# Kernel optimization log

Hardware: AMD Instinct MI355X
Metric: run time of the kernel (lower is better)

Reference implementation:

```python
import jax, jax.numpy as jnp
import numpy as np
from jax import lax

DIST_THRESH = 180.0
ATT_THRESH = 0.05


def setup_inputs() -> dict:
    key = jax.random.key(0)
    ks = jax.random.split(key, 6)
    B, N, H, W = 16, 512, 25, 25
    F, Fh = H * W, int(H * W * 1.5)  # 625, 937
    x4 = jax.random.normal(ks[0], (B, N, H, W), dtype=jnp.float32) * 0.25
    attention = jax.random.uniform(ks[1], (B, N, 1, 1), dtype=jnp.float32)
    W1 = jax.random.normal(ks[2], (2, F, Fh), dtype=jnp.float32) * (1.0 / np.sqrt(F))
    b1 = jnp.zeros((Fh,), dtype=jnp.float32)
    W2 = jax.random.normal(ks[3], (2, Fh, F), dtype=jnp.float32) * (1.0 / np.sqrt(Fh))
    b2 = jnp.zeros((F,), dtype=jnp.float32)
    return {"x4": x4, "attention": attention, "W1": W1, "b1": b1, "W2": W2, "b2": b2}


def _build_adjacency(X, att):
    """X: [B,N,F] node features, att: [B,N]. Returns thresholded adjacency [B,N,N]."""
    B, N, F = X.shape
    # pairwise L1 distances, row-by-row scan to avoid materializing [B,N,N,F]
    Xs = jnp.swapaxes(X, 0, 1)  # [N,B,F]

    def row(_, xi):  # xi: [B,F]
        d = jnp.sum(jnp.abs(xi[:, None, :] - X), axis=-1)  # [B,N]
        return None, d

    _, D = lax.scan(row, None, Xs)          # [N,B,N]
    D = jnp.swapaxes(D, 0, 1)               # [B,N,N]
    att_d = jnp.abs(att[:, :, None] - att[:, None, :])  # [B,N,N]
    A = ((D <= DIST_THRESH) & (att_d <= ATT_THRESH)).astype(jnp.float32)
    # original only fills i<j and j<i, diagonal stays 0
    A = A * (1.0 - jnp.eye(N, dtype=jnp.float32))
    return A


def _process_graph(A):
    """A + I, then row-normalize by inverse degree (D^-1 (A+I))."""
    N = A.shape[1]
    A = A + jnp.eye(N, dtype=A.dtype)
    deg = jnp.sum(A, axis=-1)               # [B,N]
    dinv = jnp.where(deg > 0, 1.0 / deg, 0.0)
    return dinv[:, :, None] * A


def _cheb_conv(x, L, Wk, b):
    """ChebConv with K=2 over dense normalized graph L: T0=x, T1=Lx."""
    t1 = jnp.einsum('bij,bjf->bif', L, x)
    return jnp.einsum('bnf,fo->bno', x, Wk[0]) + jnp.einsum('bnf,fo->bno', t1, Wk[1]) + b


def reference(x4, attention, W1, b1, W2, b2):
    B, N, H, W = x4.shape
    X = x4.reshape(B, N, H * W)             # [B,N,625] flow_x
    att = attention[:, :, 0, 0]             # [B,N]
    A = _build_adjacency(X, att)
    L = _process_graph(A)
    h = jax.nn.relu(_cheb_conv(X, L, W1, b1))   # [B,N,937]
    out = jax.nn.relu(_cheb_conv(h, L, W2, b2))  # [B,N,625]
    return out
```

## Files before the change

kernel.cpp:

```cpp
#include <hip/hip_runtime.h>
#include <stdint.h>

typedef uint16_t u16;
typedef uint32_t u32;
typedef __attribute__((ext_vector_type(4))) float f32x4;
typedef __attribute__((ext_vector_type(4))) unsigned short us4;
typedef __attribute__((ext_vector_type(8))) unsigned short us8;

#define NB   16
#define NN   512
#define FF   625
#define FH   937
#define ROWS 8192
#define KS1  1280
#define KS2  1920
#define NPX  640
#define NPH  960
#define F4   160
#define GQ   4

using frag_ab = __attribute__((ext_vector_type(8))) short;
using frag_cd = __attribute__((ext_vector_type(4))) float;

__device__ __forceinline__ u16 f32_bf16(float f) {
  union { float f; uint32_t u; } x; x.f = f;
  uint32_t r = x.u + 0x7fffu + ((x.u >> 16) & 1u);
  return (u16)(r >> 16);
}
__device__ __forceinline__ void gload_lds16(const void* g, void* l) {
  __builtin_amdgcn_global_load_lds((__attribute__((address_space(1))) void*)g,
                                   (__attribute__((address_space(3))) void*)l,
                                   16, 0, 0);
}

__global__ __launch_bounds__(256) void prep(
    const float* __restrict__ x4, const float* __restrict__ att,
    const float* __restrict__ W1, const float* __restrict__ W2,
    f32x4* __restrict__ Xpad, u16* __restrict__ Xcat, u16* __restrict__ Xt,
    u16* __restrict__ W1t, u16* __restrict__ W2t,
    u16* __restrict__ order, float* __restrict__ att_s)
{
  __shared__ __align__(16) float smem[2112];
  const int blk = blockIdx.x;
  const int tid = threadIdx.x;

  if (blk < 16) {
    float* a_sh = smem;
    const int b = blk;
    a_sh[tid]       = att[b * NN + tid];
    a_sh[tid + 256] = att[b * NN + tid + 256];
    __syncthreads();
    #pragma unroll
    for (int h = 0; h < 2; ++h) {
      const int i = tid + h * 256;
      const float ai = a_sh[i];
      int r = 0;
      for (int j = 0; j < NN; ++j) {
        const float aj = a_sh[j];
        r += (aj < ai) || (aj == ai && j < i);
      }
      order[(size_t)b * NN + r] = (u16)i;
      att_s[(size_t)b * NN + r] = ai;
    }
  } else if (blk < 1040) {
    float* T = smem;
    const int idx = blk - 16;
    const int xcd = idx & 7, sub = idx >> 3;
    const int b = xcd * 2 + (sub >> 6);
    const int rr = sub & 63;
    const int q = rr >> 4;
    const int nt = rr & 15;
    const int node0 = nt * 32;
    const int tx = tid & 31, ty = tid >> 5;
    const int lrow = tid >> 3, lcol = tid & 7;

    int buf = 0;
    {
      const int f0 = q * 160;
      #pragma unroll
      for (int r = 0; r < 4; ++r) {
        const int node = node0 + ty + r * 8;
        const int f = f0 + tx;
        T[(ty + r * 8) * 33 + tx] = (f < FF) ? x4[((size_t)b * NN + node) * FF + f] : 0.f;
      }
    }
    __syncthreads();

    for (int c = 0; c < 5; ++c) {
      const int f0 = q * 160 + c * 32;
      float vnext[4];
      const bool has = (c + 1 < 5);
      if (has) {
        const int fn = f0 + 32 + tx;
        #pragma unroll
        for (int r = 0; r < 4; ++r) {
          const int node = node0 + ty + r * 8;
          vnext[r] = (fn < FF) ? x4[((size_t)b * NN + node) * FF + fn] : 0.f;
        }
      }
      {
        const int node_l = lrow, k4s = lcol;
        const size_t grow = (size_t)b * NN + node0 + node_l;
        const int k4 = q * 40 + c * 8 + k4s;
        f32x4 v; us4 o;
        #pragma unroll
        for (int t = 0; t < 4; ++t) {
          const float x = T[buf * 1056 + node_l * 33 + k4s * 4 + t];
          v[t] = x; o[t] = f32_bf16(x);
        }
        Xpad[grow * F4 + k4] = v;
        *(us4*)(Xcat + grow * KS1 + k4 * 4) = o;
      }
      {
        const int fl = lrow, nl = lcol;
        const int f = f0 + fl;
        us4 ov;
        #pragma unroll
        for (int t = 0; t < 4; ++t)
          ov[t] = f32_bf16(T[buf * 1056 + (nl * 4 + t) * 33 + fl]);
        *(us4*)(Xt + ((size_t)b * NPX + f) * 512 + node0 + nl * 4) = ov;
      }
      if (has) {
        #pragma unroll
        for (int r = 0; r < 4; ++r)
          T[(buf ^ 1) * 1056 + (ty + r * 8) * 33 + tx] = vnext[r];
        __syncthreads();
        buf ^= 1;
      }
    }
  } else if (blk < 2320) {
    float (*tile)[33] = (float(*)[33])smem;
    const int bb = blk - 1040;
    const int kt = bb % 40, nt = bb / 40;
    const int tx = tid & 31, ty = tid >> 5;
    #pragma unroll
    for (int r = 0; r < 4; ++r) {
      int k = kt * 32 + ty + r * 8;
      int n = nt * 32 + tx;
      float v = 0.f;
      int c = -1, kk = 0;
      if (k < 625) { c = 0; kk = k; }
      else if (k >= 640 && k < 1265) { c = 1; kk = k - 640; }
      if (c >= 0 && n < FH) v = W1[((size_t)c * 625 + kk) * FH + n];
      tile[ty + r * 8][tx] = v;
    }
    __syncthreads();
    #pragma unroll
    for (int r = 0; r < 4; ++r) {
      int n = nt * 32 + ty + r * 8;
      int k = kt * 32 + tx;
      W1t[(size_t)n * KS1 + k] = f32_bf16(tile[tx][ty + r * 8]);
    }
  } else {
    float (*tile)[33] = (float(*)[33])smem;
    const int bb = blk - 2320;
    const int kt = bb % 60, nt = bb / 60;
    const int tx = tid & 31, ty = tid >> 5;
    #pragma unroll
    for (int r = 0; r < 4; ++r) {
      int k = kt * 32 + ty + r * 8;
      int n = nt * 32 + tx;
      float v = 0.f;
      int c = -1, kk = 0;
      if (k < 937) { c = 0; kk = k; }
      else if (k >= 960 && k < 1897) { c = 1; kk = k - 960; }
      if (c >= 0 && n < FF) v = W2[((size_t)c * 937 + kk) * FF + n];
      tile[ty + r * 8][tx] = v;
    }
    __syncthreads();
    #pragma unroll
    for (int r = 0; r < 4; ++r) {
      int n = nt * 32 + ty + r * 8;
      int k = kt * 32 + tx;
      W2t[(size_t)n * KS2 + k] = f32_bf16(tile[tx][ty + r * 8]);
    }
  }
}

__global__ __launch_bounds__(256) void build_L(
    const f32x4* __restrict__ Xpad,
    const u16* __restrict__ order,
    const float* __restrict__ att_s,
    u16* __restrict__ L)
{
  __shared__ float atts[512];
  __shared__ u16 ords[512];
  __shared__ u16 cand[512];
  __shared__ u16 flag[GQ][512];
  __shared__ int ncand, naccs[GQ];

  const int tid = threadIdx.x;
  const int blk = blockIdx.x;
  const int xcd = blk & 7, sub = blk >> 3;
  const int b = xcd * 2 + (sub >> 7);
  const int p0 = (sub & 127) * GQ;
  const f32x4* Xb4 = Xpad + (size_t)b * NN * F4;

  atts[tid]       = att_s[b * NN + tid];
  atts[tid + 256] = att_s[b * NN + tid + 256];
  ords[tid]       = order[b * NN + tid];
  ords[tid + 256] = order[b * NN + tid + 256];
  {
    u32* fz = (u32*)&flag[0][0];
    #pragma unroll
    for (int s = 0; s < GQ; ++s) fz[tid + s * 256] = 0;
  }
  if (tid == 0) ncand = 0;
  if (tid < GQ) naccs[tid] = 0;
  __syncthreads();

  float av[GQ]; int ig[GQ];
  #pragma unroll
  for (int g = 0; g < GQ; ++g) { av[g] = atts[p0 + g]; ig[g] = ords[p0 + g]; }
  if (tid < GQ) flag[tid][ords[p0 + tid]] = 1;

  {
    const float lo = av[0] - 0.0501f, hi = av[GQ - 1] + 0.0501f;
    const bool q0 = (atts[tid] >= lo) && (atts[tid] <= hi);
    const bool q1 = (atts[tid + 256] >= lo) && (atts[tid + 256] <= hi);
    const unsigned long long m0 = __ballot(q0);
    const unsigned long long m1 = __ballot(q1);
    const int c0 = __popcll(m0);
    const int c1 = __popcll(m1);
    const int lane = tid & 63;
    int base = 0;
    if (lane == 0 && (c0 + c1)) base = atomicAdd(&ncand, c0 + c1);
    base = __shfl(base, 0, 64);
    const unsigned long long below = (1ull << lane) - 1ull;
    if (q0) cand[base + __popcll(m0 & below)] = (u16)tid;
    if (q1) cand[base + c0 + __popcll(m1 & below)] = (u16)(tid + 256);
  }
  __syncthreads();
  const int nc = ncand;

  const int hl = tid & 31;
  const int hw = tid >> 5;

  f32x4 xi[GQ][5];
  #pragma unroll
  for (int g = 0; g < GQ; ++g) {
    const f32x4* Xi = Xb4 + (size_t)ig[g] * F4;
    #pragma unroll
    for (int s = 0; s < 5; ++s) xi[g][s] = Xi[s * 32 + hl];
  }

  for (int c = hw; c < nc; c += 8) {
    const int p = cand[c];
    const int j = ords[p];
    const float aj = atts[p];
    const f32x4* Xj = Xb4 + (size_t)j * F4;
    f32x4 xj[5];
    #pragma unroll
    for (int s = 0; s < 5; ++s) xj[s] = Xj[s * 32 + hl];

    float pd[GQ];
    #pragma unroll
    for (int g = 0; g < GQ; ++g) {
      float p2 = 0.f;
      #pragma unroll
      for (int t = 0; t < 4; ++t) {
        p2 += fabsf(xi[g][0][t] - xj[0][t]) + fabsf(xi[g][1][t] - xj[1][t])
            + fabsf(xi[g][2][t] - xj[2][t]) + fabsf(xi[g][3][t] - xj[3][t])
            + fabsf(xi[g][4][t] - xj[4][t]);
      }
      pd[g] = p2;
    }
    #pragma unroll
    for (int off = 16; off; off >>= 1) {
      #pragma unroll
      for (int g = 0; g < GQ; ++g) pd[g] += __shfl_xor(pd[g], off, 64);
    }
    if (hl == 0) {
      #pragma unroll
      for (int g = 0; g < GQ; ++g) {
        if (pd[g] <= 180.0f && fabsf(av[g] - aj) <= 0.05f && j != ig[g]) {
          flag[g][j] = 1;
          atomicAdd(&naccs[g], 1);
        }
      }
    }
  }
  __syncthreads();

  #pragma unroll
  for (int g = 0; g < GQ; ++g) {
    const u16 dv = f32_bf16(1.0f / (float)(naccs[g] + 1));
    const long row = (long)b * NN + ig[g];
    const u32 lo2 = flag[g][2 * tid]     ? (u32)dv : 0u;
    const u32 hi2 = flag[g][2 * tid + 1] ? (u32)dv : 0u;
    *(u32*)(L + (size_t)row * 512 + 2 * tid) = lo2 | (hi2 << 16);
  }
}

template <int KS, int NTILE, int NREAL, int NSTORE, bool RELU, bool BIAS, bool OUT_BF16>
__device__ __forceinline__ void gemm_core(
    const u16* __restrict__ At,
    const u16* __restrict__ Btt,
    const float* __restrict__ bias, void* __restrict__ C,
    long crow0, int col0, int ldc)
{
  constexpr int NI = NTILE / 32;
  constexpr int BR = NTILE / 32;
  __shared__ __align__(16) u16 Ash[128 * 64];
  __shared__ __align__(16) u16 Bsh[NTILE * 64];

  const int tid  = threadIdx.x;
  const int lane = tid & 63;
  const int wave = tid >> 6;
  const int wm = wave & 1, wn = wave >> 1;
  const int q = lane >> 4, l16 = lane & 15;

  const u16* pa[4]; const u16* pb[BR];
  #pragma unroll
  for (int r = 0; r < 4; ++r) {
    const int ci = r * 256 + tid;
    const int row = ci >> 3, cpos = ci & 7;
    pa[r] = At + (size_t)row * KS + (cpos ^ (row & 7)) * 8;
  }
  #pragma unroll
  for (int r = 0; r < BR; ++r) {
    const int ci = r * 256 + tid;
    const int row = ci >> 3, cpos = ci & 7;
    pb[r] = Btt + (size_t)row * KS + (cpos ^ (row & 7)) * 8;
  }
  const int wbase = (tid & 192) * 8;

  const frag_ab* fA[4][2]; const frag_ab* fB[NI][2];
  #pragma unroll
  for (int mi = 0; mi < 4; ++mi) {
    const int row = wm * 64 + mi * 16 + l16;
    fA[mi][0] = (const frag_ab*)&Ash[row * 64 + ((q    ) ^ (l16 & 7)) * 8];
    fA[mi][1] = (const frag_ab*)&Ash[row * 64 + ((q + 4) ^ (l16 & 7)) * 8];
  }
  #pragma unroll
  for (int ni = 0; ni < NI; ++ni) {
    const int row = wn * (NTILE / 2) + ni * 16 + l16;
    fB[ni][0] = (const frag_ab*)&Bsh[row * 64 + ((q    ) ^ (l16 & 7)) * 8];
    fB[ni][1] = (const frag_ab*)&Bsh[row * 64 + ((q + 4) ^ (l16 & 7)) * 8];
  }

  frag_cd acc[4][NI] = {};

  constexpr int KT = KS / 64;
  for (int kt = 0; kt < KT; ++kt) {
    __syncthreads();
    #pragma unroll
    for (int r = 0; r < 4; ++r) { gload_lds16(pa[r], &Ash[r * 2048 + wbase]); pa[r] += 64; }
    #pragma unroll
    for (int r = 0; r < BR; ++r) { gload_lds16(pb[r], &Bsh[r * 2048 + wbase]); pb[r] += 64; }
    __syncthreads();

    #pragma unroll
    for (int kk = 0; kk < 2; ++kk) {
      frag_ab av[4], bv[NI];
      #pragma unroll
      for (int mi = 0; mi < 4; ++mi) av[mi] = *fA[mi][kk];
      #pragma unroll
      for (int ni = 0; ni < NI; ++ni) bv[ni] = *fB[ni][kk];
      #pragma unroll
      for (int mi = 0; mi < 4; ++mi)
        #pragma unroll
        for (int ni = 0; ni < NI; ++ni)
          acc[mi][ni] = __builtin_amdgcn_mfma_f32_16x16x32_bf16(
              av[mi], bv[ni], acc[mi][ni], 0, 0, 0);
    }
  }

  #pragma unroll
  for (int ni = 0; ni < NI; ++ni) {
    const int col = col0 + wn * (NTILE / 2) + ni * 16 + l16;
    if (col >= NSTORE) continue;
    const bool ok = (col < NREAL);
    float bvv = 0.f;
    if (BIAS) bvv = ok ? bias[col] : 0.f;
    #pragma unroll
    for (int mi = 0; mi < 4; ++mi) {
      #pragma unroll
      for (int r = 0; r < 4; ++r) {
        const long rowg = crow0 + wm * 64 + mi * 16 + q * 4 + r;
        float v = acc[mi][ni][r];
        if (BIAS) v += bvv;
        if (RELU) v = fmaxf(v, 0.f);
        if (!ok) v = 0.f;
        if (OUT_BF16) ((u16*)C)[rowg * (size_t)ldc + col] = f32_bf16(v);
        else          ((float*)C)[rowg * (size_t)ldc + col] = v;
      }
    }
  }
}

template <int KS, int NTILE, int NREAL, int NSTORE, bool RELU, bool BIAS, bool OUT_BF16>
__global__ __launch_bounds__(256) void gemm_dense(
    const u16* __restrict__ A, const u16* __restrict__ Bt,
    const float* __restrict__ bias, void* __restrict__ C, int ldc)
{
  const int x = blockIdx.x;
  const int mt = ((x & 7) << 3) | (x >> 3);
  gemm_core<KS, NTILE, NREAL, NSTORE, RELU, BIAS, OUT_BF16>(
      A + (size_t)mt * 128 * KS, Bt + (size_t)blockIdx.y * NTILE * KS,
      bias, C, (long)mt * 128, blockIdx.y * NTILE, ldc);
}

template <int NP>
__global__ __launch_bounds__(256) void spmm(
    const u16* __restrict__ L, const u16* __restrict__ Bt,
    u16* __restrict__ C, int ldc)
{
  constexpr int TPB = 4 * (NP / 64);
  const int blk = blockIdx.x;
  const int xcd = blk & 7, sub = blk >> 3;
  const int b = xcd * 2 + sub / TPB;
  const int t = sub % TPB;
  const int mt = t & 3, nt = t >> 2;
  gemm_core<512, 64, NP, NP, false, false, true>(
      L + ((size_t)b * 512 + mt * 128) * 512,
      Bt + ((size_t)b * NP + nt * 64) * 512,
      nullptr, C, (long)b * 512 + mt * 128, nt * 64, ldc);
}

__global__ __launch_bounds__(256) void transpose_h(
    const u16* __restrict__ hcat, u16* __restrict__ ht)
{
  __shared__ u16 tile[32][34];
  const int blk = blockIdx.x;
  const int xcd = blk & 7, sub = blk >> 3;
  const int b = xcd * 2 + sub / 480;
  const int t = sub % 480;
  const int kt = t % 16, nt = t / 16;
  const int tid = threadIdx.x;
  const int tx = tid & 31, ty = tid >> 5;
  #pragma unroll
  for (int r = 0; r < 4; ++r) {
    const int node = kt * 32 + ty + r * 8;
    const int n = nt * 32 + tx;
    tile[ty + r * 8][tx] = hcat[((size_t)b * NN + node) * KS2 + n];
  }
  __syncthreads();
  #pragma unroll
  for (int r = 0; r < 4; ++r) {
    const int n = nt * 32 + ty + r * 8;
    const int node = kt * 32 + tx;
    ht[((size_t)b * NPH + n) * 512 + node] = tile[tx][ty + r * 8];
  }
}

extern "C" void kernel_launch(void* const* d_in, const int* in_sizes, int n_in,
                              void* d_out, int out_size, void* d_ws, size_t ws_size,
                              hipStream_t stream) {
  const float* x4  = (const float*)d_in[0];
  const float* att = (const float*)d_in[1];
  const float* W1  = (const float*)d_in[2];
  const float* b1  = (const float*)d_in[3];
  const float* W2  = (const float*)d_in[4];
  const float* b2  = (const float*)d_in[5];
  float* out = (float*)d_out;

  char* ws = (char*)d_ws;
  f32x4* Xpad = (f32x4*)ws;
  u16* ht = (u16*)ws;       ws += (size_t)ROWS * F4 * 16;
  u16* Xcat = (u16*)ws;  ws += (size_t)ROWS * KS1 * 2;
  u16* hcat = (u16*)ws;  ws += (size_t)ROWS * KS2 * 2;
  u16* W1t  = (u16*)ws;  ws += (size_t)1024 * KS1 * 2;
  u16* W2t  = (u16*)ws;  ws += (size_t)640 * KS2 * 2;
  u16* Lm   = (u16*)ws;  ws += (size_t)NB * 512 * 512 * 2;
  u16* Xt   = (u16*)ws;  ws += (size_t)NB * NPX * 512 * 2;
  float* att_s = (float*)ws; ws += (size_t)NB * NN * 4;
  u16* order_  = (u16*)ws;   ws += (size_t)NB * NN * 2;

  prep<<<dim3(3520), 256, 0, stream>>>(x4, att, W1, W2, Xpad, Xcat, Xt,
                                       W1t, W2t, order_, att_s);
  build_L<<<dim3(2048), 256, 0, stream>>>(Xpad, order_, att_s, Lm);
  spmm<NPX><<<dim3(640), 256, 0, stream>>>(Lm, Xt, Xcat + NPX, KS1);
  gemm_dense<KS1, 128, FH, NPH, true, true, true><<<dim3(64, 8), 256, 0, stream>>>(
      Xcat, W1t, b1, (void*)hcat, KS2);
  transpose_h<<<dim3(7680), 256, 0, stream>>>(hcat, ht);
  spmm<NPH><<<dim3(960), 256, 0, stream>>>(Lm, ht, hcat + NPH, KS2);
  gemm_dense<KS2, 64, FF, FF, true, true, false><<<dim3(64, 10), 256, 0, stream>>>(
      hcat, W2t, b2, (void*)out, FF);
}
```

Before: 221.8 us.

## Fuse transpose into first dense GEMM epilogue and retile second-layer GEMMs

```diff
diff --git a/kernel.cpp b/kernel.cpp
--- a/kernel.cpp
+++ b/kernel.cpp
@@ -292,11 +292,13 @@
   }
 }
 
-template <int KS, int NTILE, int NREAL, int NSTORE, bool RELU, bool BIAS, bool OUT_BF16>
+template <int KS, int NTILE, int NREAL, int NSTORE, bool RELU, bool BIAS,
+          bool OUT_BF16, bool WT>
 __device__ __forceinline__ void gemm_core(
     const u16* __restrict__ At,
     const u16* __restrict__ Btt,
     const float* __restrict__ bias, void* __restrict__ C,
+    u16* __restrict__ Ct,
     long crow0, int col0, int ldc)
 {
   constexpr int NI = NTILE / 32;
@@ -375,6 +377,7 @@
     if (BIAS) bvv = ok ? bias[col] : 0.f;
     #pragma unroll
     for (int mi = 0; mi < 4; ++mi) {
+      us4 tv;
       #pragma unroll
       for (int r = 0; r < 4; ++r) {
         const long rowg = crow0 + wm * 64 + mi * 16 + q * 4 + r;
@@ -382,66 +385,52 @@
         if (BIAS) v += bvv;
         if (RELU) v = fmaxf(v, 0.f);
         if (!ok) v = 0.f;
-        if (OUT_BF16) ((u16*)C)[rowg * (size_t)ldc + col] = f32_bf16(v);
-        else          ((float*)C)[rowg * (size_t)ldc + col] = v;
-      }
-    }
-  }
-}
-
-template <int KS, int NTILE, int NREAL, int NSTORE, bool RELU, bool BIAS, bool OUT_BF16>
+        if (OUT_BF16) {
+          const u16 v16 = f32_bf16(v);
+          ((u16*)C)[rowg * (size_t)ldc + col] = v16;
+          if (WT) tv[r] = v16;
+        } else {
+          ((float*)C)[rowg * (size_t)ldc + col] = v;
+        }
+      }
+      if (WT) {
+        const long bb = crow0 >> 9;
+        const int node = (int)(crow0 & 511) + wm * 64 + mi * 16 + q * 4;
+        *(us4*)(Ct + ((size_t)bb * NPH + col) * 512 + node) = tv;
+      }
+    }
+  }
+}
+
+template <int KS, int NTILE, int NREAL, int NSTORE, bool RELU, bool BIAS,
+          bool OUT_BF16, bool WT>
 __global__ __launch_bounds__(256) void gemm_dense(
     const u16* __restrict__ A, const u16* __restrict__ Bt,
-    const float* __restrict__ bias, void* __restrict__ C, int ldc)
+    const float* __restrict__ bias, void* __restrict__ C,
+    u16* __restrict__ Ct, int ldc)
 {
   const int x = blockIdx.x;
   const int mt = ((x & 7) << 3) | (x >> 3);
-  gemm_core<KS, NTILE, NREAL, NSTORE, RELU, BIAS, OUT_BF16>(
+  gemm_core<KS, NTILE, NREAL, NSTORE, RELU, BIAS, OUT_BF16, WT>(
       A + (size_t)mt * 128 * KS, Bt + (size_t)blockIdx.y * NTILE * KS,
-      bias, C, (long)mt * 128, blockIdx.y * NTILE, ldc);
-}
-
-template <int NP>
+      bias, C, Ct, (long)mt * 128, blockIdx.y * NTILE, ldc);
+}
+
+template <int NP, int NT>
 __global__ __launch_bounds__(256) void spmm(
     const u16* __restrict__ L, const u16* __restrict__ Bt,
     u16* __restrict__ C, int ldc)
 {
-  constexpr int TPB = 4 * (NP / 64);
+  constexpr int TPB = 4 * (NP / NT);
   const int blk = blockIdx.x;
   const int xcd = blk & 7, sub = blk >> 3;
   const int b = xcd * 2 + sub / TPB;
   const int t = sub % TPB;
   const int mt = t & 3, nt = t >> 2;
-  gemm_core<512, 64, NP, NP, false, false, true>(
+  gemm_core<512, NT, NP, NP, false, false, true, false>(
       L + ((size_t)b * 512 + mt * 128) * 512,
-      Bt + ((size_t)b * NP + nt * 64) * 512,
-      nullptr, C, (long)b * 512 + mt * 128, nt * 64, ldc);
-}
-
-__global__ __launch_bounds__(256) void transpose_h(
-    const u16* __restrict__ hcat, u16* __restrict__ ht)
-{
-  __shared__ u16 tile[32][34];
-  const int blk = blockIdx.x;
-  const int xcd = blk & 7, sub = blk >> 3;
-  const int b = xcd * 2 + sub / 480;
-  const int t = sub % 480;
-  const int kt = t % 16, nt = t / 16;
-  const int tid = threadIdx.x;
-  const int tx = tid & 31, ty = tid >> 5;
-  #pragma unroll
-  for (int r = 0; r < 4; ++r) {
-    const int node = kt * 32 + ty + r * 8;
-    const int n = nt * 32 + tx;
-    tile[ty + r * 8][tx] = hcat[((size_t)b * NN + node) * KS2 + n];
-  }
-  __syncthreads();
-  #pragma unroll
-  for (int r = 0; r < 4; ++r) {
-    const int n = nt * 32 + ty + r * 8;
-    const int node = kt * 32 + tx;
-    ht[((size_t)b * NPH + n) * 512 + node] = tile[tx][ty + r * 8];
-  }
+      Bt + ((size_t)b * NP + nt * NT) * 512,
+      nullptr, C, nullptr, (long)b * 512 + mt * 128, nt * NT, ldc);
 }
 
 extern "C" void kernel_launch(void* const* d_in, const int* in_sizes, int n_in,
@@ -470,11 +459,10 @@
   prep<<<dim3(3520), 256, 0, stream>>>(x4, att, W1, W2, Xpad, Xcat, Xt,
                                        W1t, W2t, order_, att_s);
   build_L<<<dim3(2048), 256, 0, stream>>>(Xpad, order_, att_s, Lm);
-  spmm<NPX><<<dim3(640), 256, 0, stream>>>(Lm, Xt, Xcat + NPX, KS1);
-  gemm_dense<KS1, 128, FH, NPH, true, true, true><<<dim3(64, 8), 256, 0, stream>>>(
-      Xcat, W1t, b1, (void*)hcat, KS2);
-  transpose_h<<<dim3(7680), 256, 0, stream>>>(hcat, ht);
-  spmm<NPH><<<dim3(960), 256, 0, stream>>>(Lm, ht, hcat + NPH, KS2);
-  gemm_dense<KS2, 64, FF, FF, true, true, false><<<dim3(64, 10), 256, 0, stream>>>(
-      hcat, W2t, b2, (void*)out, FF);
-}
+  spmm<NPX, 64><<<dim3(640), 256, 0, stream>>>(Lm, Xt, Xcat + NPX, KS1);
+  gemm_dense<KS1, 128, FH, NPH, true, true, true, true><<<dim3(64, 8), 256, 0, stream>>>(
+      Xcat, W1t, b1, (void*)hcat, ht, KS2);
+  spmm<NPH, 96><<<dim3(640), 256, 0, stream>>>(Lm, ht, hcat + NPH, KS2);
+  gemm_dense<KS2, 96, FF, FF, true, true, false, false><<<dim3(64, 7), 256, 0, stream>>>(
+      hcat, W2t, b2, (void*)out, nullptr, FF);
+}
```

Result: no change. 222.9 us (+0.5%).
